# Kernel optimization log

Hardware: AMD Instinct MI355X
Metric: run time of the kernel (lower is better)

## Reference

```python
import jax, jax.numpy as jnp
import numpy as np

B, W, S, D, H = 16, 128, 16, 768, 12
HD = D // H

def _ln(x, g, b):
    m = x.mean(-1, keepdims=True)
    v = ((x - m) ** 2).mean(-1, keepdims=True)
    return (x - m) / jnp.sqrt(v + 1e-5) * g + b

def _lin(x, w, b):
    return x @ w.T + b

def _rope(t):
    # t: (N, H, L, HD); interleaved even/odd rotation, base 10000
    inv = 1.0 / (10000.0 ** (jnp.arange(0, HD, 2, dtype=jnp.float32) / HD))
    fr = jnp.arange(t.shape[2], dtype=jnp.float32)[:, None] * inv[None, :]  # (L, HD//2)
    cos, sin = jnp.cos(fr), jnp.sin(fr)
    te, to = t[..., ::2], t[..., 1::2]
    return jnp.stack([te * cos - to * sin, te * sin + to * cos], -1).reshape(t.shape)

def _mha(q, k, v, mask=None):
    # q,k,v: (N, H, L, HD)
    s = jnp.einsum('nhqd,nhkd->nhqk', q, k) / jnp.sqrt(jnp.float32(HD))
    if mask is not None:
        s = jnp.where(mask[None, None], -jnp.inf, s)
    a = jax.nn.softmax(s, axis=-1)
    return jnp.einsum('nhqk,nhkd->nhqd', a, v)

def _heads(t, L):
    return t.reshape(-1, L, H, HD).transpose(0, 2, 1, 3)

def setup_inputs() -> dict:
    key = jax.random.key(0)
    ks = jax.random.split(key, 16)
    def w(i, shape):
        return jax.random.normal(ks[i], shape, jnp.float32) * 0.02
    return {
        'x': jax.random.normal(ks[0], (B, W, S, D), jnp.float32),
        'causal_mask': jnp.triu(jnp.ones((W, W), dtype=bool), k=1),
        'sn_g': jnp.ones((D,), jnp.float32), 'sn_b': jnp.zeros((D,), jnp.float32),
        'sa_in_w': w(1, (3 * D, D)), 'sa_in_b': jnp.zeros((3 * D,), jnp.float32),
        'sa_out_w': w(2, (D, D)), 'sa_out_b': jnp.zeros((D,), jnp.float32),
        'tn_g': jnp.ones((D,), jnp.float32), 'tn_b': jnp.zeros((D,), jnp.float32),
        'tq_w': w(3, (D, D)), 'tq_b': jnp.zeros((D,), jnp.float32),
        'tk_w': w(4, (D, D)), 'tk_b': jnp.zeros((D,), jnp.float32),
        'tv_w': w(5, (D, D)), 'tv_b': jnp.zeros((D,), jnp.float32),
        'to_w': w(6, (D, D)), 'to_b': jnp.zeros((D,), jnp.float32),
        'fn_g': jnp.ones((D,), jnp.float32), 'fn_b': jnp.zeros((D,), jnp.float32),
        'f1_w': w(7, (4 * D, D)), 'f1_b': jnp.zeros((4 * D,), jnp.float32),
        'f2_w': w(8, (D, 4 * D)), 'f2_b': jnp.zeros((D,), jnp.float32),
    }

def reference(x, causal_mask, sn_g, sn_b, sa_in_w, sa_in_b, sa_out_w, sa_out_b,
              tn_g, tn_b, tq_w, tq_b, tk_w, tk_b, tv_w, tv_b, to_w, to_b,
              fn_g, fn_b, f1_w, f1_b, f2_w, f2_b):
    # ---- spatial attention within each timestep: (B*W, S, D) ----
    xs = x.reshape(B * W, S, D)
    xn = _ln(xs, sn_g, sn_b)
    q, k, v = jnp.split(_lin(xn, sa_in_w, sa_in_b), 3, axis=-1)
    o = _mha(_heads(q, S), _heads(k, S), _heads(v, S))
    o = o.transpose(0, 2, 1, 3).reshape(B * W, S, D)
    xs = xs + _lin(o, sa_out_w, sa_out_b)
    x = xs.reshape(B, W, S, D)
    # ---- causal temporal attention with RoPE: (B*S, W, D) ----
    xt = x.transpose(0, 2, 1, 3).reshape(B * S, W, D)
    xn = _ln(xt, tn_g, tn_b)
    q = _rope(_heads(_lin(xn, tq_w, tq_b), W))
    k = _rope(_heads(_lin(xn, tk_w, tk_b), W))
    v = _heads(_lin(xn, tv_w, tv_b), W)
    o = _mha(q, k, v, causal_mask)
    o = o.transpose(0, 2, 1, 3).reshape(B * S, W, D)
    xt = xt + _lin(o, to_w, to_b)
    x = xt.reshape(B, S, W, D).transpose(0, 2, 1, 3)
    # ---- feed-forward (exact GELU, as torch default) ----
    h = jax.nn.gelu(_lin(_ln(x, fn_g, fn_b), f1_w, f1_b), approximate=False)
    return x + _lin(h, f2_w, f2_b)
```

## Files before the change

kernel.cpp:

```cpp
#include <hip/hip_runtime.h>
#include <stdint.h>


#define NB 16
#define NW 128
#define NS 16
#define ND 768
#define NH 12
#define NTOK 32768

typedef __attribute__((ext_vector_type(8))) short short8;
typedef __attribute__((ext_vector_type(4))) float f32x4;

__device__ __forceinline__ float blo(unsigned v){ return __builtin_bit_cast(float, v << 16); }
__device__ __forceinline__ float bhi(unsigned v){ return __builtin_bit_cast(float, v & 0xffff0000u); }
__device__ __forceinline__ float bus(unsigned short u){ return __builtin_bit_cast(float, ((unsigned)u) << 16); }
__device__ __forceinline__ unsigned short f2b(float f){
  unsigned u = __builtin_bit_cast(unsigned, f);
  u += 0x7fffu + ((u >> 16) & 1u);
  return (unsigned short)(u >> 16);
}
__device__ __forceinline__ void gld_lds16(const void* g, void* l){
  __builtin_amdgcn_global_load_lds((const __attribute__((address_space(1))) void*)g,
                                   (__attribute__((address_space(3))) void*)l, 16, 0, 0);
}

__global__ __launch_bounds__(256) void convertall_k(
    const float* __restrict__ s0, const float* __restrict__ s1, const float* __restrict__ s2,
    const float* __restrict__ s3, const float* __restrict__ s4, const float* __restrict__ s5,
    const float* __restrict__ s6, const float* __restrict__ s7,
    unsigned short* __restrict__ d0, unsigned short* __restrict__ d1, unsigned short* __restrict__ d2,
    unsigned short* __restrict__ d3, unsigned short* __restrict__ d4, unsigned short* __restrict__ d5,
    unsigned short* __restrict__ d6, unsigned short* __restrict__ d7){
  const int n0 = 442368, n1 = 147456, n2 = 147456, n3 = 147456, n4 = 147456, n5 = 147456, n6 = 589824, n7 = 589824;
  const int c0 = n0, c1 = c0+n1, c2 = c1+n2, c3 = c2+n3, c4 = c3+n4, c5 = c4+n5, c6 = c5+n6, c7 = c6+n7;
  int i = blockIdx.x * 256 + threadIdx.x;
  const int stride = gridDim.x * 256;
  for (; i < c7; i += stride){
    const float* s; unsigned short* d; int j;
    if      (i < c0){ s = s0; d = d0; j = i; }
    else if (i < c1){ s = s1; d = d1; j = i - c0; }
    else if (i < c2){ s = s2; d = d2; j = i - c1; }
    else if (i < c3){ s = s3; d = d3; j = i - c2; }
    else if (i < c4){ s = s4; d = d4; j = i - c3; }
    else if (i < c5){ s = s5; d = d5; j = i - c4; }
    else if (i < c6){ s = s6; d = d6; j = i - c5; }
    else            { s = s7; d = d7; j = i - c6; }
    float4 v = ((const float4*)s)[j];
    unsigned lo = (unsigned)f2b(v.x) | ((unsigned)f2b(v.y) << 16);
    unsigned hi = (unsigned)f2b(v.z) | ((unsigned)f2b(v.w) << 16);
    ((uint2*)d)[j] = make_uint2(lo, hi);
  }
}

__global__ __launch_bounds__(256) void concat3_k(const float* __restrict__ a, const float* __restrict__ b,
                                                 const float* __restrict__ c, float* __restrict__ o){
  int i = blockIdx.x * 256 + threadIdx.x;
  if (i < 768){ o[i] = a[i]; o[768 + i] = b[i]; o[1536 + i] = c[i]; }
}

__global__ __launch_bounds__(256) void rope_k(float* __restrict__ tab){
  int i = blockIdx.x * 256 + threadIdx.x;
  if (i < 128 * 32){
    int w = i >> 5, p = i & 31;
    float inv = powf(10000.0f, -((float)(2 * p)) / 64.0f);
    float ang = (float)w * inv;
    tab[i * 2] = cosf(ang);
    tab[i * 2 + 1] = sinf(ang);
  }
}

template<int INF32>
__global__ __launch_bounds__(256) void ln_k(const void* __restrict__ xin, const float* __restrict__ g,
                                            const float* __restrict__ bt, unsigned short* __restrict__ out){
  const int row = blockIdx.x;
  const int t = threadIdx.x;
  const float* xf = (const float*)xin;
  const unsigned short* xb = (const unsigned short*)xin;
  float v[3];
#pragma unroll
  for (int i = 0; i < 3; ++i){
    int j = t + i * 256;
    v[i] = INF32 ? xf[(size_t)row * 768 + j] : bus(xb[(size_t)row * 768 + j]);
  }
  float s = v[0] + v[1] + v[2];
  float ss = v[0]*v[0] + v[1]*v[1] + v[2]*v[2];
#pragma unroll
  for (int o = 1; o < 64; o <<= 1){ s += __shfl_xor(s, o, 64); ss += __shfl_xor(ss, o, 64); }
  __shared__ float red[8];
  int w = t >> 6;
  if ((t & 63) == 0){ red[w*2] = s; red[w*2+1] = ss; }
  __syncthreads();
  s = red[0] + red[2] + red[4] + red[6];
  ss = red[1] + red[3] + red[5] + red[7];
  float mean = s * (1.0f / 768.0f);
  float var = ss * (1.0f / 768.0f) - mean * mean;
  float rstd = rsqrtf(var + 1e-5f);
#pragma unroll
  for (int i = 0; i < 3; ++i){
    int j = t + i * 256;
    out[(size_t)row * 768 + j] = f2b((v[i] - mean) * rstd * g[j] + bt[j]);
  }
}

template<int MODE>
__global__ __launch_bounds__(256, 4) void gemm97_k(const unsigned short* __restrict__ A,
                                                   const unsigned short* __restrict__ Bw,
                                                   const float* __restrict__ bias,
                                                   const void* __restrict__ resid,
                                                   void* __restrict__ outp, int K, int M){
  __shared__ char LB[16384];
  char* const As = LB;
  char* const Bs = LB + 8192;
  const int tid = threadIdx.x;
  const int lane = tid & 63, w = tid >> 6;
  const int llo = lane & 15, lhi = lane >> 4;
  const int wm = w >> 1, wn = w & 1;
  const int NT = K >> 5;

  const int gx = gridDim.x, gy = gridDim.y;
  const int nwg = gx * gy;
  const int orig = blockIdx.y * gx + blockIdx.x;
  int bxx, byy;
  if (((nwg & 7) == 0) && ((gy & 63) == 0)){
    const int xcd = orig & 7, idx = orig >> 3;
    const int grpsz = gx << 3;
    const int g = idx / grpsz, rem = idx - g * grpsz;
    bxx = rem >> 3;
    byy = xcd * (gy >> 3) + (g << 3) + (rem & 7);
  } else {
    byy = orig / gx; bxx = orig - byy * gx;
  }
  const int brow = byy << 7;
  const int bcol = bxx << 7;

  const int lineb = tid >> 3, cfb = tid & 7;
  const int cfs = cfb ^ (lineb & 7);
  const int srow = 2 * lineb + (cfs >> 2);
  const int skc = cfs & 3;
  const char* pa = (const char*)(A + (size_t)(brow + srow) * K + skc * 8);
  const char* pb = (const char*)(Bw + (size_t)(bcol + srow) * K + skc * 8);
  const int rowJ = K * 128;
  const int ldst = w << 10;

  int aoff[4], boff[4];
#pragma unroll
  for (int mi = 0; mi < 4; ++mi){
    const int rr = (wm << 6) + (mi << 4) + llo;
    const int line = rr >> 1;
    const int pos = ((((rr & 1) << 2) | lhi)) ^ (line & 7);
    aoff[mi] = line * 128 + pos * 16;
  }
#pragma unroll
  for (int ni = 0; ni < 4; ++ni){
    const int cc = (wn << 6) + (ni << 4) + llo;
    const int line = cc >> 1;
    const int pos = ((((cc & 1) << 2) | lhi)) ^ (line & 7);
    boff[ni] = line * 128 + pos * 16;
  }

  f32x4 acc[4][4];
#pragma unroll
  for (int m = 0; m < 4; ++m)
#pragma unroll
    for (int n = 0; n < 4; ++n) acc[m][n] = f32x4{0.f, 0.f, 0.f, 0.f};

  for (int t = 0; t < NT; ++t){
    gld_lds16(pa,        As + ldst);
    gld_lds16(pa + rowJ, As + ldst + 4096);
    gld_lds16(pb,        Bs + ldst);
    gld_lds16(pb + rowJ, Bs + ldst + 4096);
    pa += 64; pb += 64;
    __syncthreads();
    short8 a[4], b[4];
#pragma unroll
    for (int i = 0; i < 4; ++i){
      a[i] = *(const short8*)(As + aoff[i]);
      b[i] = *(const short8*)(Bs + boff[i]);
    }
    __builtin_amdgcn_s_setprio(1);
#pragma unroll
    for (int mi = 0; mi < 4; ++mi)
#pragma unroll
      for (int ni = 0; ni < 4; ++ni)
        acc[mi][ni] = __builtin_amdgcn_mfma_f32_16x16x32_bf16(b[ni], a[mi], acc[mi][ni], 0, 0, 0);
    __builtin_amdgcn_s_setprio(0);
    __syncthreads();
  }

  const int orow = brow + (wm << 6);
  const int ocol = bcol + (wn << 6);
  const unsigned short* resb = (const unsigned short*)resid;
  const float* resf = (const float*)resid;
#pragma unroll
  for (int m = 0; m < 4; ++m){
    const int row = orow + (m << 4) + llo;
    const size_t rb = (size_t)row * M;
#pragma unroll
    for (int n = 0; n < 4; ++n){
      const int col = ocol + (n << 4) + (lhi << 2);
      const float4 bv = *(const float4*)&bias[col];
      float v0 = acc[m][n][0] + bv.x;
      float v1 = acc[m][n][1] + bv.y;
      float v2 = acc[m][n][2] + bv.z;
      float v3 = acc[m][n][3] + bv.w;
      const size_t off = rb + col;
      if (MODE == 1){
        float y0 = v0 * (1.5957691216f + 0.0713548163f * v0 * v0);
        float y1 = v1 * (1.5957691216f + 0.0713548163f * v1 * v1);
        float y2 = v2 * (1.5957691216f + 0.0713548163f * v2 * v2);
        float y3 = v3 * (1.5957691216f + 0.0713548163f * v3 * v3);
        v0 = v0 / (1.0f + __expf(-y0));
        v1 = v1 / (1.0f + __expf(-y1));
        v2 = v2 / (1.0f + __expf(-y2));
        v3 = v3 / (1.0f + __expf(-y3));
      } else if (MODE == 2){
        const float4 rv = *(const float4*)&resf[off];
        v0 += rv.x; v1 += rv.y; v2 += rv.z; v3 += rv.w;
      } else if (MODE == 3 || MODE == 4){
        const uint2 rv = *(const uint2*)&resb[off];
        v0 += blo(rv.x); v1 += bhi(rv.x); v2 += blo(rv.y); v3 += bhi(rv.y);
      }
      if (MODE == 4){
        float4 ov; ov.x = v0; ov.y = v1; ov.z = v2; ov.w = v3;
        *(float4*)&((float*)outp)[off] = ov;
      } else {
        unsigned lo = (unsigned)f2b(v0) | ((unsigned)f2b(v1) << 16);
        unsigned hi = (unsigned)f2b(v2) | ((unsigned)f2b(v3) << 16);
        *(uint2*)&((unsigned short*)outp)[off] = make_uint2(lo, hi);
      }
    }
  }
}

__global__ __launch_bounds__(256) void sattn_k(const unsigned short* __restrict__ qkv,
                                               unsigned short* __restrict__ o){
  const int bw = blockIdx.x, h = blockIdx.y;
  const int t = threadIdx.x;
  __shared__ unsigned short qh[16 * 68], kh[16 * 68], vh[16 * 68];
  __shared__ float pl[16 * 17];
  const int row = t >> 4, c4 = t & 15;
  const size_t base = ((size_t)(bw * 16 + row)) * 2304 + h * 64 + c4 * 4;
  *(uint2*)&qh[row * 68 + c4 * 4] = *(const uint2*)&qkv[base];
  *(uint2*)&kh[row * 68 + c4 * 4] = *(const uint2*)&qkv[base + 768];
  *(uint2*)&vh[row * 68 + c4 * 4] = *(const uint2*)&qkv[base + 1536];
  __syncthreads();

  const int q = row, k = c4;
  float s = 0.f;
#pragma unroll
  for (int c = 0; c < 16; ++c){
    uint2 qv = *(const uint2*)&qh[q * 68 + c * 4];
    uint2 kv = *(const uint2*)&kh[k * 68 + c * 4];
    s += blo(qv.x) * blo(kv.x) + bhi(qv.x) * bhi(kv.x);
    s += blo(qv.y) * blo(kv.y) + bhi(qv.y) * bhi(kv.y);
  }
  s *= 0.125f;
  float m = s;
#pragma unroll
  for (int off = 1; off < 16; off <<= 1) m = fmaxf(m, __shfl_xor(m, off, 64));
  float p = __expf(s - m);
  float su = p;
#pragma unroll
  for (int off = 1; off < 16; off <<= 1) su += __shfl_xor(su, off, 64);
  pl[q * 17 + k] = p / su;
  __syncthreads();

  float o0 = 0.f, o1 = 0.f, o2 = 0.f, o3 = 0.f;
#pragma unroll
  for (int kk = 0; kk < 16; ++kk){
    float pw = pl[q * 17 + kk];
    uint2 vv = *(const uint2*)&vh[kk * 68 + c4 * 4];
    o0 += pw * blo(vv.x); o1 += pw * bhi(vv.x);
    o2 += pw * blo(vv.y); o3 += pw * bhi(vv.y);
  }
  const size_t ob = ((size_t)(bw * 16 + q)) * 768 + h * 64 + c4 * 4;
  unsigned r0 = (unsigned)f2b(o0) | ((unsigned)f2b(o1) << 16);
  unsigned r1 = (unsigned)f2b(o2) | ((unsigned)f2b(o3) << 16);
  *(uint2*)&o[ob] = make_uint2(r0, r1);
}

__global__ __launch_bounds__(256) void tattn_k(const unsigned short* __restrict__ qkv,
                                               const float* __restrict__ rope,
                                               unsigned short* __restrict__ o){
  const int bs = blockIdx.x, h = blockIdx.y;
  const int b = bs >> 4, s = bs & 15;
  const int t = threadIdx.x, lane = t & 63, w = t >> 6;
  const int lhi = lane >> 4, llo = lane & 15;
  __shared__ unsigned short Qs[128 * 64];
  __shared__ unsigned short Ks[128 * 64];
  __shared__ unsigned short Vt[64 * 128];
  __shared__ unsigned short P[128 * 128];

  {
    const int r = t >> 1;
    const int dbase = (t & 1) * 32;
    const size_t tokb = ((size_t)((b * 128 + r) * 16 + s)) * 2304 + h * 64;
    const float2* rp = (const float2*)rope;
#pragma unroll
    for (int mch = 0; mch < 4; ++mch){
      const int d0 = dbase + mch * 8;
      uint4 qv = *(const uint4*)&qkv[tokb + d0];
      uint4 kv = *(const uint4*)&qkv[tokb + 768 + d0];
      uint4 vv = *(const uint4*)&qkv[tokb + 1536 + d0];
      unsigned qin[4] = {qv.x, qv.y, qv.z, qv.w};
      unsigned kin[4] = {kv.x, kv.y, kv.z, kv.w};
      unsigned qo[4], ko[4];
#pragma unroll
      for (int j = 0; j < 4; ++j){
        float2 cssn = rp[r * 32 + (d0 >> 1) + j];
        float cs = cssn.x, sn = cssn.y;
        float qe = blo(qin[j]), qd = bhi(qin[j]);
        float ke = blo(kin[j]), kd = bhi(kin[j]);
        qo[j] = (unsigned)f2b(qe * cs - qd * sn) | ((unsigned)f2b(qe * sn + qd * cs) << 16);
        ko[j] = (unsigned)f2b(ke * cs - kd * sn) | ((unsigned)f2b(ke * sn + kd * cs) << 16);
      }
      const int byq = r * 128 + ((d0 * 2) ^ ((r & 7) << 4));
      *(uint4*)((char*)Qs + byq) = make_uint4(qo[0], qo[1], qo[2], qo[3]);
      *(uint4*)((char*)Ks + byq) = make_uint4(ko[0], ko[1], ko[2], ko[3]);
      unsigned vin[4] = {vv.x, vv.y, vv.z, vv.w};
#pragma unroll
      for (int j = 0; j < 8; ++j){
        const int d = d0 + j;
        unsigned short val = (j & 1) ? (unsigned short)(vin[j >> 1] >> 16)
                                     : (unsigned short)(vin[j >> 1] & 0xffffu);
        *(unsigned short*)((char*)Vt + d * 256 + ((r * 2) ^ ((d & 7) << 4))) = val;
      }
    }
  }
  __syncthreads();

  const int qbase = w * 32;
  f32x4 st[8][2];
#pragma unroll
  for (int i = 0; i < 8; ++i){ st[i][0] = f32x4{0.f,0.f,0.f,0.f}; st[i][1] = f32x4{0.f,0.f,0.f,0.f}; }
#pragma unroll
  for (int kd = 0; kd < 2; ++kd){
    short8 bq[2];
#pragma unroll
    for (int fq = 0; fq < 2; ++fq){
      const int qr = qbase + fq * 16 + llo;
      bq[fq] = *(const short8*)((const char*)Qs + qr * 128 + ((kd * 64 + lhi * 16) ^ ((qr & 7) << 4)));
    }
#pragma unroll
    for (int fk = 0; fk < 8; ++fk){
      const int kr = fk * 16 + llo;
      short8 ak = *(const short8*)((const char*)Ks + kr * 128 + ((kd * 64 + lhi * 16) ^ ((kr & 7) << 4)));
      st[fk][0] = __builtin_amdgcn_mfma_f32_16x16x32_bf16(ak, bq[0], st[fk][0], 0, 0, 0);
      st[fk][1] = __builtin_amdgcn_mfma_f32_16x16x32_bf16(ak, bq[1], st[fk][1], 0, 0, 0);
    }
  }

#pragma unroll
  for (int fq = 0; fq < 2; ++fq){
    const int qg = qbase + fq * 16 + llo;
    float m = -1e30f;
#pragma unroll
    for (int fk = 0; fk < 8; ++fk)
#pragma unroll
      for (int rr = 0; rr < 4; ++rr){
        const int kg = fk * 16 + lhi * 4 + rr;
        float sv = (kg <= qg) ? st[fk][fq][rr] : -1e30f;
        st[fk][fq][rr] = sv;
        m = fmaxf(m, sv);
      }
    m = fmaxf(m, __shfl_xor(m, 16, 64));
    m = fmaxf(m, __shfl_xor(m, 32, 64));
    float su = 0.f;
#pragma unroll
    for (int fk = 0; fk < 8; ++fk)
#pragma unroll
      for (int rr = 0; rr < 4; ++rr){
        float p = __expf((st[fk][fq][rr] - m) * 0.125f);
        st[fk][fq][rr] = p;
        su += p;
      }
    su += __shfl_xor(su, 16, 64);
    su += __shfl_xor(su, 32, 64);
    const float rs = 1.0f / su;
#pragma unroll
    for (int fk = 0; fk < 8; ++fk){
      const int kk = fk * 16 + lhi * 4;
      unsigned lo = (unsigned)f2b(st[fk][fq][0] * rs) | ((unsigned)f2b(st[fk][fq][1] * rs) << 16);
      unsigned hi = (unsigned)f2b(st[fk][fq][2] * rs) | ((unsigned)f2b(st[fk][fq][3] * rs) << 16);
      *(uint2*)((char*)P + qg * 256 + ((kk * 2) ^ ((qg & 7) << 4))) = make_uint2(lo, hi);
    }
  }
  __syncthreads();

  f32x4 oacc[2][4];
#pragma unroll
  for (int i = 0; i < 2; ++i)
#pragma unroll
    for (int j = 0; j < 4; ++j) oacc[i][j] = f32x4{0.f,0.f,0.f,0.f};
#pragma unroll
  for (int ks = 0; ks < 4; ++ks){
    short8 pa[2];
#pragma unroll
    for (int fq = 0; fq < 2; ++fq){
      const int qr = qbase + fq * 16 + llo;
      pa[fq] = *(const short8*)((const char*)P + qr * 256 + ((ks * 64 + lhi * 16) ^ ((qr & 7) << 4)));
    }
#pragma unroll
    for (int fd = 0; fd < 4; ++fd){
      const int dr = fd * 16 + llo;
      short8 vb = *(const short8*)((const char*)Vt + dr * 256 + ((ks * 64 + lhi * 16) ^ ((dr & 7) << 4)));
      oacc[0][fd] = __builtin_amdgcn_mfma_f32_16x16x32_bf16(pa[0], vb, oacc[0][fd], 0, 0, 0);
      oacc[1][fd] = __builtin_amdgcn_mfma_f32_16x16x32_bf16(pa[1], vb, oacc[1][fd], 0, 0, 0);
    }
  }

#pragma unroll
  for (int fq = 0; fq < 2; ++fq)
#pragma unroll
    for (int fd = 0; fd < 4; ++fd)
#pragma unroll
      for (int rr = 0; rr < 4; ++rr){
        const int qg = qbase + fq * 16 + lhi * 4 + rr;
        const int d = fd * 16 + llo;
        const size_t ob = ((size_t)((b * 128 + qg) * 16 + s)) * 768 + h * 64 + d;
        o[ob] = f2b(oacc[fq][fd][rr]);
      }
}

__global__ __launch_bounds__(256) void sentinel_k(float* out){
  if (blockIdx.x == 0 && threadIdx.x == 0) out[0] = 12345.0f;
}

extern "C" void kernel_launch(void* const* d_in, const int* in_sizes, int n_in,
                              void* d_out, int out_size, void* d_ws, size_t ws_size,
                              hipStream_t stream){
  const float* x       = (const float*)d_in[0];
  const float* sn_g    = (const float*)d_in[2];
  const float* sn_b    = (const float*)d_in[3];
  const float* sa_in_w = (const float*)d_in[4];
  const float* sa_in_b = (const float*)d_in[5];
  const float* sa_out_w= (const float*)d_in[6];
  const float* sa_out_b= (const float*)d_in[7];
  const float* tn_g    = (const float*)d_in[8];
  const float* tn_b    = (const float*)d_in[9];
  const float* tq_w    = (const float*)d_in[10];
  const float* tq_b    = (const float*)d_in[11];
  const float* tk_w    = (const float*)d_in[12];
  const float* tk_b    = (const float*)d_in[13];
  const float* tv_w    = (const float*)d_in[14];
  const float* tv_b    = (const float*)d_in[15];
  const float* to_w    = (const float*)d_in[16];
  const float* to_b    = (const float*)d_in[17];
  const float* fn_g    = (const float*)d_in[18];
  const float* fn_b    = (const float*)d_in[19];
  const float* f1_w    = (const float*)d_in[20];
  const float* f1_b    = (const float*)d_in[21];
  const float* f2_w    = (const float*)d_in[22];
  const float* f2_b    = (const float*)d_in[23];

  char* ws = (char*)d_ws;
  size_t off = 0;
  auto alloc = [&](size_t bytes) -> void* {
    void* p = ws + off;
    off += (bytes + 255) & ~(size_t)255;
    return p;
  };
  unsigned short* Wqkv = (unsigned short*)alloc((size_t)2304*768*2);
  unsigned short* Wo1  = (unsigned short*)alloc((size_t)768*768*2);
  unsigned short* W3   = (unsigned short*)alloc((size_t)2304*768*2);
  float*          b3   = (float*)alloc(2304*4);
  unsigned short* Wto  = (unsigned short*)alloc((size_t)768*768*2);
  unsigned short* Wf1  = (unsigned short*)alloc((size_t)3072*768*2);
  unsigned short* Wf2  = (unsigned short*)alloc((size_t)768*3072*2);
  float*          rope = (float*)alloc(128*32*2*4);
  unsigned short* xn   = (unsigned short*)alloc((size_t)NTOK*768*2);
  unsigned short* qkv  = (unsigned short*)alloc((size_t)NTOK*3072*2);
  unsigned short* xs2  = (unsigned short*)alloc((size_t)NTOK*768*2);
  unsigned short* xt2  = (unsigned short*)alloc((size_t)NTOK*768*2);
  unsigned short* ob   = xn;

  if (ws_size < off){ sentinel_k<<<1, 64, 0, stream>>>((float*)d_out); return; }

  convertall_k<<<2048, 256, 0, stream>>>(sa_in_w, sa_out_w, tq_w, tk_w, tv_w, to_w, f1_w, f2_w,
                                         Wqkv, Wo1, W3, W3 + 768*768, W3 + 2*768*768, Wto, Wf1, Wf2);
  concat3_k<<<3, 256, 0, stream>>>(tq_b, tk_b, tv_b, b3);
  rope_k<<<16, 256, 0, stream>>>(rope);

  ln_k<1><<<NTOK, 256, 0, stream>>>(x, sn_g, sn_b, xn);
  gemm97_k<0><<<dim3(18, 256), 256, 0, stream>>>(xn, Wqkv, sa_in_b, nullptr, qkv, 768, 2304);
  sattn_k<<<dim3(2048, 12), 256, 0, stream>>>(qkv, ob);
  gemm97_k<2><<<dim3(6, 256), 256, 0, stream>>>(ob, Wo1, sa_out_b, x, xs2, 768, 768);

  ln_k<0><<<NTOK, 256, 0, stream>>>(xs2, tn_g, tn_b, xn);
  gemm97_k<0><<<dim3(18, 256), 256, 0, stream>>>(xn, W3, b3, nullptr, qkv, 768, 2304);
  tattn_k<<<dim3(256, 12), 256, 0, stream>>>(qkv, rope, ob);
  gemm97_k<3><<<dim3(6, 256), 256, 0, stream>>>(ob, Wto, to_b, xs2, xt2, 768, 768);

  ln_k<0><<<NTOK, 256, 0, stream>>>(xt2, fn_g, fn_b, xn);
  gemm97_k<1><<<dim3(24, 256), 256, 0, stream>>>(xn, Wf1, f1_b, nullptr, qkv, 768, 3072);
  gemm97_k<4><<<dim3(6, 256), 256, 0, stream>>>(qkv, Wf2, f2_b, xt2, d_out, 3072, 768);
}
```

Baseline: 1.111 ms.

## Pre-pack weights in MFMA fragment order and load B directly from global

Weights are now converted into a packed layout that matches the MFMA B-fragment order, so each wave reads its B operands straight from global memory (through cache) instead of staging them in LDS. The A tile uses double-buffered LDS with explicit vmcnt waits and raw barriers, and each wave now owns a 32x128 output strip instead of 64x64. This is meant to remove B-tile LDS traffic and overlap the A loads with compute. In exchange, every wave re-reads B from L2 each k-step, and the weight conversion grows from one launch to eight.

```diff
diff --git a/kernel.cpp b/kernel.cpp
--- a/kernel.cpp
+++ b/kernel.cpp
@@ -25,32 +25,26 @@
                                    (__attribute__((address_space(3))) void*)l, 16, 0, 0);
 }
 
-__global__ __launch_bounds__(256) void convertall_k(
-    const float* __restrict__ s0, const float* __restrict__ s1, const float* __restrict__ s2,
-    const float* __restrict__ s3, const float* __restrict__ s4, const float* __restrict__ s5,
-    const float* __restrict__ s6, const float* __restrict__ s7,
-    unsigned short* __restrict__ d0, unsigned short* __restrict__ d1, unsigned short* __restrict__ d2,
-    unsigned short* __restrict__ d3, unsigned short* __restrict__ d4, unsigned short* __restrict__ d5,
-    unsigned short* __restrict__ d6, unsigned short* __restrict__ d7){
-  const int n0 = 442368, n1 = 147456, n2 = 147456, n3 = 147456, n4 = 147456, n5 = 147456, n6 = 589824, n7 = 589824;
-  const int c0 = n0, c1 = c0+n1, c2 = c1+n2, c3 = c2+n3, c4 = c3+n4, c5 = c4+n5, c6 = c5+n6, c7 = c6+n7;
-  int i = blockIdx.x * 256 + threadIdx.x;
-  const int stride = gridDim.x * 256;
-  for (; i < c7; i += stride){
-    const float* s; unsigned short* d; int j;
-    if      (i < c0){ s = s0; d = d0; j = i; }
-    else if (i < c1){ s = s1; d = d1; j = i - c0; }
-    else if (i < c2){ s = s2; d = d2; j = i - c1; }
-    else if (i < c3){ s = s3; d = d3; j = i - c2; }
-    else if (i < c4){ s = s4; d = d4; j = i - c3; }
-    else if (i < c5){ s = s5; d = d5; j = i - c4; }
-    else if (i < c6){ s = s6; d = d6; j = i - c5; }
-    else            { s = s7; d = d7; j = i - c6; }
-    float4 v = ((const float4*)s)[j];
-    unsigned lo = (unsigned)f2b(v.x) | ((unsigned)f2b(v.y) << 16);
-    unsigned hi = (unsigned)f2b(v.z) | ((unsigned)f2b(v.w) << 16);
-    ((uint2*)d)[j] = make_uint2(lo, hi);
-  }
+__global__ __launch_bounds__(256) void pack_k(const float* __restrict__ src,
+                                              unsigned short* __restrict__ dst,
+                                              int K, int NTk, int nch){
+  int c = blockIdx.x * 256 + threadIdx.x;
+  if (c >= nch) return;
+  const int lane = c & 63;
+  const int ni = (c >> 6) & 7;
+  const int rest = c >> 9;
+  const int t = rest % NTk;
+  const int cb = rest / NTk;
+  const int m = cb * 128 + ni * 16 + (lane & 15);
+  const int k0 = t * 32 + (lane >> 4) * 8;
+  const float* s = src + (size_t)m * K + k0;
+  float4 v0 = *(const float4*)s;
+  float4 v1 = *(const float4*)(s + 4);
+  unsigned p0 = (unsigned)f2b(v0.x) | ((unsigned)f2b(v0.y) << 16);
+  unsigned p1 = (unsigned)f2b(v0.z) | ((unsigned)f2b(v0.w) << 16);
+  unsigned p2 = (unsigned)f2b(v1.x) | ((unsigned)f2b(v1.y) << 16);
+  unsigned p3 = (unsigned)f2b(v1.z) | ((unsigned)f2b(v1.w) << 16);
+  ((uint4*)dst)[c] = make_uint4(p0, p1, p2, p3);
 }
 
 __global__ __launch_bounds__(256) void concat3_k(const float* __restrict__ a, const float* __restrict__ b,
@@ -104,18 +98,15 @@
 }
 
 template<int MODE>
-__global__ __launch_bounds__(256, 4) void gemm97_k(const unsigned short* __restrict__ A,
-                                                   const unsigned short* __restrict__ Bw,
+__global__ __launch_bounds__(256, 4) void gemmbd_k(const unsigned short* __restrict__ A,
+                                                   const unsigned short* __restrict__ Bp,
                                                    const float* __restrict__ bias,
                                                    const void* __restrict__ resid,
                                                    void* __restrict__ outp, int K, int M){
-  __shared__ char LB[16384];
-  char* const As = LB;
-  char* const Bs = LB + 8192;
+  __shared__ char As[16384];
   const int tid = threadIdx.x;
   const int lane = tid & 63, w = tid >> 6;
   const int llo = lane & 15, lhi = lane >> 4;
-  const int wm = w >> 1, wn = w & 1;
   const int NT = K >> 5;
 
   const int gx = gridDim.x, gy = gridDim.y;
@@ -139,66 +130,72 @@
   const int srow = 2 * lineb + (cfs >> 2);
   const int skc = cfs & 3;
   const char* pa = (const char*)(A + (size_t)(brow + srow) * K + skc * 8);
-  const char* pb = (const char*)(Bw + (size_t)(bcol + srow) * K + skc * 8);
   const int rowJ = K * 128;
   const int ldst = w << 10;
 
-  int aoff[4], boff[4];
-#pragma unroll
-  for (int mi = 0; mi < 4; ++mi){
-    const int rr = (wm << 6) + (mi << 4) + llo;
+  const char* gB = (const char*)Bp + (size_t)bxx * K * 256 + lane * 16;
+
+  int aoff[2];
+#pragma unroll
+  for (int mi = 0; mi < 2; ++mi){
+    const int rr = (w << 5) + (mi << 4) + llo;
     const int line = rr >> 1;
     const int pos = ((((rr & 1) << 2) | lhi)) ^ (line & 7);
     aoff[mi] = line * 128 + pos * 16;
   }
-#pragma unroll
-  for (int ni = 0; ni < 4; ++ni){
-    const int cc = (wn << 6) + (ni << 4) + llo;
-    const int line = cc >> 1;
-    const int pos = ((((cc & 1) << 2) | lhi)) ^ (line & 7);
-    boff[ni] = line * 128 + pos * 16;
-  }
-
-  f32x4 acc[4][4];
-#pragma unroll
-  for (int m = 0; m < 4; ++m)
-#pragma unroll
-    for (int n = 0; n < 4; ++n) acc[m][n] = f32x4{0.f, 0.f, 0.f, 0.f};
+
+  f32x4 acc[2][8];
+#pragma unroll
+  for (int m = 0; m < 2; ++m)
+#pragma unroll
+    for (int n = 0; n < 8; ++n) acc[m][n] = f32x4{0.f, 0.f, 0.f, 0.f};
+
+  gld_lds16(pa,        As + ldst);
+  gld_lds16(pa + rowJ, As + ldst + 4096);
+  pa += 64;
 
   for (int t = 0; t < NT; ++t){
-    gld_lds16(pa,        As + ldst);
-    gld_lds16(pa + rowJ, As + ldst + 4096);
-    gld_lds16(pb,        Bs + ldst);
-    gld_lds16(pb + rowJ, Bs + ldst + 4096);
-    pa += 64; pb += 64;
-    __syncthreads();
-    short8 a[4], b[4];
-#pragma unroll
-    for (int i = 0; i < 4; ++i){
-      a[i] = *(const short8*)(As + aoff[i]);
-      b[i] = *(const short8*)(Bs + boff[i]);
-    }
+    if (t + 1 < NT){
+      char* dst = As + (((t + 1) & 1) << 13) + ldst;
+      gld_lds16(pa,        dst);
+      gld_lds16(pa + rowJ, dst + 4096);
+      pa += 64;
+      asm volatile("s_waitcnt vmcnt(2)" ::: "memory");
+    } else {
+      asm volatile("s_waitcnt vmcnt(0)" ::: "memory");
+    }
+    __builtin_amdgcn_s_barrier();
+
+    const char* gBt = gB + (size_t)t * 8192;
+    short8 b[8];
+#pragma unroll
+    for (int ni = 0; ni < 8; ++ni)
+      b[ni] = *(const short8*)(gBt + ni * 1024);
+
+    const char* Ab = As + ((t & 1) << 13);
+    short8 a0 = *(const short8*)(Ab + aoff[0]);
+    short8 a1 = *(const short8*)(Ab + aoff[1]);
+
     __builtin_amdgcn_s_setprio(1);
 #pragma unroll
-    for (int mi = 0; mi < 4; ++mi)
-#pragma unroll
-      for (int ni = 0; ni < 4; ++ni)
-        acc[mi][ni] = __builtin_amdgcn_mfma_f32_16x16x32_bf16(b[ni], a[mi], acc[mi][ni], 0, 0, 0);
+    for (int ni = 0; ni < 8; ++ni){
+      acc[0][ni] = __builtin_amdgcn_mfma_f32_16x16x32_bf16(b[ni], a0, acc[0][ni], 0, 0, 0);
+      acc[1][ni] = __builtin_amdgcn_mfma_f32_16x16x32_bf16(b[ni], a1, acc[1][ni], 0, 0, 0);
+    }
     __builtin_amdgcn_s_setprio(0);
-    __syncthreads();
-  }
-
-  const int orow = brow + (wm << 6);
-  const int ocol = bcol + (wn << 6);
+    __builtin_amdgcn_s_barrier();
+  }
+
+  const int orow = brow + (w << 5);
   const unsigned short* resb = (const unsigned short*)resid;
   const float* resf = (const float*)resid;
 #pragma unroll
-  for (int m = 0; m < 4; ++m){
+  for (int m = 0; m < 2; ++m){
     const int row = orow + (m << 4) + llo;
     const size_t rb = (size_t)row * M;
 #pragma unroll
-    for (int n = 0; n < 4; ++n){
-      const int col = ocol + (n << 4) + (lhi << 2);
+    for (int n = 0; n < 8; ++n){
+      const int col = bcol + (n << 4) + (lhi << 2);
       const float4 bv = *(const float4*)&bias[col];
       float v0 = acc[m][n][0] + bv.x;
       float v1 = acc[m][n][1] + bv.y;
@@ -477,22 +474,28 @@
 
   if (ws_size < off){ sentinel_k<<<1, 64, 0, stream>>>((float*)d_out); return; }
 
-  convertall_k<<<2048, 256, 0, stream>>>(sa_in_w, sa_out_w, tq_w, tk_w, tv_w, to_w, f1_w, f2_w,
-                                         Wqkv, Wo1, W3, W3 + 768*768, W3 + 2*768*768, Wto, Wf1, Wf2);
+  pack_k<<<864, 256, 0, stream>>>(sa_in_w, Wqkv, 768, 24, 2304*768/8);
+  pack_k<<<288, 256, 0, stream>>>(sa_out_w, Wo1, 768, 24, 768*768/8);
+  pack_k<<<288, 256, 0, stream>>>(tq_w, W3, 768, 24, 768*768/8);
+  pack_k<<<288, 256, 0, stream>>>(tk_w, W3 + 768*768, 768, 24, 768*768/8);
+  pack_k<<<288, 256, 0, stream>>>(tv_w, W3 + 2*768*768, 768, 24, 768*768/8);
+  pack_k<<<288, 256, 0, stream>>>(to_w, Wto, 768, 24, 768*768/8);
+  pack_k<<<1152, 256, 0, stream>>>(f1_w, Wf1, 768, 24, 3072*768/8);
+  pack_k<<<1152, 256, 0, stream>>>(f2_w, Wf2, 3072, 96, 768*3072/8);
   concat3_k<<<3, 256, 0, stream>>>(tq_b, tk_b, tv_b, b3);
   rope_k<<<16, 256, 0, stream>>>(rope);
 
   ln_k<1><<<NTOK, 256, 0, stream>>>(x, sn_g, sn_b, xn);
-  gemm97_k<0><<<dim3(18, 256), 256, 0, stream>>>(xn, Wqkv, sa_in_b, nullptr, qkv, 768, 2304);
+  gemmbd_k<0><<<dim3(18, 256), 256, 0, stream>>>(xn, Wqkv, sa_in_b, nullptr, qkv, 768, 2304);
   sattn_k<<<dim3(2048, 12), 256, 0, stream>>>(qkv, ob);
-  gemm97_k<2><<<dim3(6, 256), 256, 0, stream>>>(ob, Wo1, sa_out_b, x, xs2, 768, 768);
+  gemmbd_k<2><<<dim3(6, 256), 256, 0, stream>>>(ob, Wo1, sa_out_b, x, xs2, 768, 768);
 
   ln_k<0><<<NTOK, 256, 0, stream>>>(xs2, tn_g, tn_b, xn);
-  gemm97_k<0><<<dim3(18, 256), 256, 0, stream>>>(xn, W3, b3, nullptr, qkv, 768, 2304);
+  gemmbd_k<0><<<dim3(18, 256), 256, 0, stream>>>(xn, W3, b3, nullptr, qkv, 768, 2304);
   tattn_k<<<dim3(256, 12), 256, 0, stream>>>(qkv, rope, ob);
-  gemm97_k<3><<<dim3(6, 256), 256, 0, stream>>>(ob, Wto, to_b, xs2, xt2, 768, 768);
+  gemmbd_k<3><<<dim3(6, 256), 256, 0, stream>>>(ob, Wto, to_b, xs2, xt2, 768, 768);
 
   ln_k<0><<<NTOK, 256, 0, stream>>>(xt2, fn_g, fn_b, xn);
-  gemm97_k<1><<<dim3(24, 256), 256, 0, stream>>>(xn, Wf1, f1_b, nullptr, qkv, 768, 3072);
-  gemm97_k<4><<<dim3(6, 256), 256, 0, stream>>>(qkv, Wf2, f2_b, xt2, d_out, 3072, 768);
-}
+  gemmbd_k<1><<<dim3(24, 256), 256, 0, stream>>>(xn, Wf1, f1_b, nullptr, qkv, 768, 3072);
+  gemmbd_k<4><<<dim3(6, 256), 256, 0, stream>>>(qkv, Wf2, f2_b, xt2, d_out, 3072, 768);
+}
```

New measurement: 1.339 ms. 1.21x slower.

## Replace 128x128 GEMM with 256x256 double-buffered LDS tiled kernel

Applied to the files above, without the earlier changes.

Replaces the GEMM used by all projections with a 512-thread kernel computing 256x256 output tiles over K-steps of 64, double-buffering the A/B tiles in 128KB of LDS so the next tile is fetched while MFMAs run on the current one. Each wave now accumulates a 128x64 sub-tile, raising operand reuse and halving barriers per K element. It also simplifies the XCD-aware block remapping. The trade is much higher LDS and register use, limiting occupancy to about one block per CU, and fewer blocks for the N=768 GEMMs, which can leave CUs idle in the tail.

```diff
diff --git a/kernel.cpp b/kernel.cpp
--- a/kernel.cpp
+++ b/kernel.cpp
@@ -104,96 +104,98 @@
 }
 
 template<int MODE>
-__global__ __launch_bounds__(256, 4) void gemm97_k(const unsigned short* __restrict__ A,
-                                                   const unsigned short* __restrict__ Bw,
-                                                   const float* __restrict__ bias,
-                                                   const void* __restrict__ resid,
-                                                   void* __restrict__ outp, int K, int M){
-  __shared__ char LB[16384];
-  char* const As = LB;
-  char* const Bs = LB + 8192;
+__global__ __launch_bounds__(512, 2) void gemm256_k(const unsigned short* __restrict__ A,
+                                                    const unsigned short* __restrict__ Bw,
+                                                    const float* __restrict__ bias,
+                                                    const void* __restrict__ resid,
+                                                    void* __restrict__ outp, int K, int M){
+  __shared__ char LB[131072];
+  char* const Abuf = LB;
+  char* const Bbuf = LB + 65536;
   const int tid = threadIdx.x;
   const int lane = tid & 63, w = tid >> 6;
   const int llo = lane & 15, lhi = lane >> 4;
-  const int wm = w >> 1, wn = w & 1;
-  const int NT = K >> 5;
-
-  const int gx = gridDim.x, gy = gridDim.y;
-  const int nwg = gx * gy;
+  const int wm = w >> 2, wn = w & 3;
+  const int NT = K >> 6;
+
+  const int gx = gridDim.x;
+  const int nwg = gx * gridDim.y;
   const int orig = blockIdx.y * gx + blockIdx.x;
-  int bxx, byy;
-  if (((nwg & 7) == 0) && ((gy & 63) == 0)){
-    const int xcd = orig & 7, idx = orig >> 3;
-    const int grpsz = gx << 3;
-    const int g = idx / grpsz, rem = idx - g * grpsz;
-    bxx = rem >> 3;
-    byy = xcd * (gy >> 3) + (g << 3) + (rem & 7);
-  } else {
-    byy = orig / gx; bxx = orig - byy * gx;
-  }
-  const int brow = byy << 7;
-  const int bcol = bxx << 7;
-
-  const int lineb = tid >> 3, cfb = tid & 7;
-  const int cfs = cfb ^ (lineb & 7);
-  const int srow = 2 * lineb + (cfs >> 2);
-  const int skc = cfs & 3;
-  const char* pa = (const char*)(A + (size_t)(brow + srow) * K + skc * 8);
-  const char* pb = (const char*)(Bw + (size_t)(bcol + srow) * K + skc * 8);
+  const int lin = (nwg & 7) ? orig : ((orig & 7) * (nwg >> 3) + (orig >> 3));
+  const int by = lin / gx, bx = lin - by * gx;
+  const int brow = by << 8;
+  const int bcol = bx << 8;
+
+  const int r0 = tid >> 3, cp = tid & 7;
+  const int swz = (cp << 4) ^ ((r0 & 7) << 4);
+  const char* aG = (const char*)(A + (size_t)(brow + r0) * K) + swz;
+  const char* bG = (const char*)(Bw + (size_t)(bcol + r0) * K) + swz;
   const int rowJ = K * 128;
   const int ldst = w << 10;
 
-  int aoff[4], boff[4];
-#pragma unroll
-  for (int mi = 0; mi < 4; ++mi){
-    const int rr = (wm << 6) + (mi << 4) + llo;
-    const int line = rr >> 1;
-    const int pos = ((((rr & 1) << 2) | lhi)) ^ (line & 7);
-    aoff[mi] = line * 128 + pos * 16;
-  }
-#pragma unroll
-  for (int ni = 0; ni < 4; ++ni){
-    const int cc = (wn << 6) + (ni << 4) + llo;
-    const int line = cc >> 1;
-    const int pos = ((((cc & 1) << 2) | lhi)) ^ (line & 7);
-    boff[ni] = line * 128 + pos * 16;
-  }
-
-  f32x4 acc[4][4];
-#pragma unroll
-  for (int m = 0; m < 4; ++m)
+  auto stage = [&](const char* g, int gb, char* buf){
+#pragma unroll
+    for (int j = 0; j < 4; ++j)
+      gld_lds16(g + gb + j * rowJ, buf + ldst + j * 8192);
+  };
+
+  f32x4 acc[8][4];
+#pragma unroll
+  for (int m = 0; m < 8; ++m)
 #pragma unroll
     for (int n = 0; n < 4; ++n) acc[m][n] = f32x4{0.f, 0.f, 0.f, 0.f};
 
+  stage(aG, 0, Abuf);
+  stage(bG, 0, Bbuf);
+  asm volatile("s_waitcnt vmcnt(0)" ::: "memory");
+  __builtin_amdgcn_s_barrier();
+
   for (int t = 0; t < NT; ++t){
-    gld_lds16(pa,        As + ldst);
-    gld_lds16(pa + rowJ, As + ldst + 4096);
-    gld_lds16(pb,        Bs + ldst);
-    gld_lds16(pb + rowJ, Bs + ldst + 4096);
-    pa += 64; pb += 64;
-    __syncthreads();
-    short8 a[4], b[4];
-#pragma unroll
-    for (int i = 0; i < 4; ++i){
-      a[i] = *(const short8*)(As + aoff[i]);
-      b[i] = *(const short8*)(Bs + boff[i]);
-    }
-    __builtin_amdgcn_s_setprio(1);
-#pragma unroll
-    for (int mi = 0; mi < 4; ++mi)
-#pragma unroll
-      for (int ni = 0; ni < 4; ++ni)
-        acc[mi][ni] = __builtin_amdgcn_mfma_f32_16x16x32_bf16(b[ni], a[mi], acc[mi][ni], 0, 0, 0);
-    __builtin_amdgcn_s_setprio(0);
-    __syncthreads();
-  }
-
-  const int orow = brow + (wm << 6);
+    if (t + 1 < NT){
+      stage(aG, (t + 1) << 7, Abuf + (((t + 1) & 1) << 15));
+      stage(bG, (t + 1) << 7, Bbuf + (((t + 1) & 1) << 15));
+    }
+    const char* Ab = Abuf + ((t & 1) << 15);
+    const char* Bb = Bbuf + ((t & 1) << 15);
+
+    short8 b[4][2];
+#pragma unroll
+    for (int ni = 0; ni < 4; ++ni){
+      const int cc = (wn << 6) + (ni << 4) + llo;
+#pragma unroll
+      for (int ks = 0; ks < 2; ++ks)
+        b[ni][ks] = *(const short8*)(Bb + cc * 128 + (((ks << 6) + (lhi << 4)) ^ ((cc & 7) << 4)));
+    }
+#pragma unroll
+    for (int mh = 0; mh < 2; ++mh){
+      short8 a[4][2];
+#pragma unroll
+      for (int mi = 0; mi < 4; ++mi){
+        const int rr = (wm << 7) + (mh << 6) + (mi << 4) + llo;
+#pragma unroll
+        for (int ks = 0; ks < 2; ++ks)
+          a[mi][ks] = *(const short8*)(Ab + rr * 128 + (((ks << 6) + (lhi << 4)) ^ ((rr & 7) << 4)));
+      }
+      __builtin_amdgcn_s_setprio(1);
+#pragma unroll
+      for (int mi = 0; mi < 4; ++mi)
+#pragma unroll
+        for (int ni = 0; ni < 4; ++ni){
+          acc[mh * 4 + mi][ni] = __builtin_amdgcn_mfma_f32_16x16x32_bf16(b[ni][0], a[mi][0], acc[mh * 4 + mi][ni], 0, 0, 0);
+          acc[mh * 4 + mi][ni] = __builtin_amdgcn_mfma_f32_16x16x32_bf16(b[ni][1], a[mi][1], acc[mh * 4 + mi][ni], 0, 0, 0);
+        }
+      __builtin_amdgcn_s_setprio(0);
+    }
+    asm volatile("s_waitcnt vmcnt(0)" ::: "memory");
+    __builtin_amdgcn_s_barrier();
+  }
+
+  const int orow = brow + (wm << 7);
   const int ocol = bcol + (wn << 6);
   const unsigned short* resb = (const unsigned short*)resid;
   const float* resf = (const float*)resid;
 #pragma unroll
-  for (int m = 0; m < 4; ++m){
+  for (int m = 0; m < 8; ++m){
     const int row = orow + (m << 4) + llo;
     const size_t rb = (size_t)row * M;
 #pragma unroll
@@ -483,16 +485,16 @@
   rope_k<<<16, 256, 0, stream>>>(rope);
 
   ln_k<1><<<NTOK, 256, 0, stream>>>(x, sn_g, sn_b, xn);
-  gemm97_k<0><<<dim3(18, 256), 256, 0, stream>>>(xn, Wqkv, sa_in_b, nullptr, qkv, 768, 2304);
+  gemm256_k<0><<<dim3(9, 128), 512, 0, stream>>>(xn, Wqkv, sa_in_b, nullptr, qkv, 768, 2304);
   sattn_k<<<dim3(2048, 12), 256, 0, stream>>>(qkv, ob);
-  gemm97_k<2><<<dim3(6, 256), 256, 0, stream>>>(ob, Wo1, sa_out_b, x, xs2, 768, 768);
+  gemm256_k<2><<<dim3(3, 128), 512, 0, stream>>>(ob, Wo1, sa_out_b, x, xs2, 768, 768);
 
   ln_k<0><<<NTOK, 256, 0, stream>>>(xs2, tn_g, tn_b, xn);
-  gemm97_k<0><<<dim3(18, 256), 256, 0, stream>>>(xn, W3, b3, nullptr, qkv, 768, 2304);
+  gemm256_k<0><<<dim3(9, 128), 512, 0, stream>>>(xn, W3, b3, nullptr, qkv, 768, 2304);
   tattn_k<<<dim3(256, 12), 256, 0, stream>>>(qkv, rope, ob);
-  gemm97_k<3><<<dim3(6, 256), 256, 0, stream>>>(ob, Wto, to_b, xs2, xt2, 768, 768);
+  gemm256_k<3><<<dim3(3, 128), 512, 0, stream>>>(ob, Wto, to_b, xs2, xt2, 768, 768);
 
   ln_k<0><<<NTOK, 256, 0, stream>>>(xt2, fn_g, fn_b, xn);
-  gemm97_k<1><<<dim3(24, 256), 256, 0, stream>>>(xn, Wf1, f1_b, nullptr, qkv, 768, 3072);
-  gemm97_k<4><<<dim3(6, 256), 256, 0, stream>>>(qkv, Wf2, f2_b, xt2, d_out, 3072, 768);
-}
+  gemm256_k<1><<<dim3(12, 128), 512, 0, stream>>>(xn, Wf1, f1_b, nullptr, qkv, 768, 3072);
+  gemm256_k<4><<<dim3(3, 128), 512, 0, stream>>>(qkv, Wf2, f2_b, xt2, d_out, 3072, 768);
+}
```

Result: faster. 1.087 ms (-2.1%).
